# Optimization experiments

Measured on AMD Instinct MI355X. Metric: run time of the kernel, lower is better.

Reference implementation:

```python
import jax, jax.numpy as jnp
import numpy as np

N, T = 32, 1024
CIN, H, O, F2 = 64, 128, 16, 16  # F2 = 2 * FiLMed_layers
EPS = 1e-5
SLOPE = 0.01  # nn.LeakyReLU default


def _leaky(x):
    return jnp.where(x >= 0, x, SLOPE * x)


def _ln(x, gamma, beta):
    # x: (N,T,O,H); gamma,beta: (O,H) -> broadcast per channel
    mu = jnp.mean(x, axis=-1, keepdims=True)
    var = jnp.mean(jnp.square(x - mu), axis=-1, keepdims=True)
    return (x - mu) * jax.lax.rsqrt(var + EPS) * gamma + beta


def setup_inputs() -> dict:
    key = jax.random.key(0)
    ks = jax.random.split(key, 7)
    s0 = 1.0 / np.sqrt(CIN)
    s1 = 1.0 / np.sqrt(H)
    return {
        "x": jax.random.normal(ks[0], (N, T, CIN), jnp.float32),
        "W0": jax.random.uniform(ks[1], (O, H, CIN), jnp.float32, -s0, s0),
        "b0": jax.random.uniform(ks[2], (O, H), jnp.float32, -s0, s0),
        "g0": jnp.ones((O, H), jnp.float32),
        "be0": jnp.zeros((O, H), jnp.float32),
        "W1": jax.random.uniform(ks[3], (O, H, H), jnp.float32, -s1, s1),
        "b1": jax.random.uniform(ks[4], (O, H), jnp.float32, -s1, s1),
        "g1": jnp.ones((O, H), jnp.float32),
        "be1": jnp.zeros((O, H), jnp.float32),
        "W2": jax.random.uniform(ks[5], (O, F2, H), jnp.float32, -s1, s1),
        "b2": jax.random.uniform(ks[6], (O, F2), jnp.float32, -s1, s1),
    }


def reference(x, W0, b0, g0, be0, W1, b1, g1, be1, W2, b2):
    # Per-channel MLP, vectorized over the O channel axis.
    h = jnp.einsum("ntc,ohc->ntoh", x, W0) + b0          # (N,T,O,H)
    h = _ln(_leaky(h), g0, be0)
    h = jnp.einsum("ntoh,ogh->ntog", h, W1) + b1         # (N,T,O,H)
    h = _ln(_leaky(h), g1, be1)
    out = jnp.einsum("ntoh,ofh->ntof", h, W2) + b2       # (N,T,O,F2)
    out = _leaky(out)
    # torch: stack(dim=1) -> (N,O,T,F2); moveaxis(1,-1) -> (N,T,F2,O)
    return jnp.moveaxis(out, 2, 3)
```

## Files before the change

### kernel.cpp

```cpp
#include <hip/hip_runtime.h>
#include <hip/hip_bf16.h>

#define NTOK  32768
#define CIN   64
#define HDIM  128
#define O_CH  16
#define F2    16
#define SLOPE 0.01f
#define EPS   1e-5f

#define SW0_STRIDE 72
#define SW1_STRIDE 136
#define SW2_STRIDE 136
#define SH_STRIDE  136
#define SW0_OFF 0
#define SW1_OFF 9216
#define SW2_OFF (9216 + 17408)
#define WIMG_SHORTS 28800
#define SH_OFF  28800
#define SH_ROWS 256
#define SBIAS_OFF (SH_OFF + SH_ROWS * SH_STRIDE)
#define SBIAS_FLOATS 272
#define SMEM_SHORTS (SBIAS_OFF + SBIAS_FLOATS * 2)

#define WIMG_OFF   0
#define WIMG_BYTES ((size_t)O_CH * WIMG_SHORTS * 2)
#define B0F_OFF    WIMG_BYTES
#define B0F_BYTES  ((size_t)O_CH * HDIM * 4)
#define B1F_OFF    (B0F_OFF + B0F_BYTES)
#define B1F_BYTES  ((size_t)O_CH * HDIM * 4)
#define B2F_OFF    (B1F_OFF + B1F_BYTES)

typedef __attribute__((ext_vector_type(8))) short bf16x8;
typedef __attribute__((ext_vector_type(4))) short bf16x4;
typedef __attribute__((ext_vector_type(4))) float f32x4;

__device__ __forceinline__ unsigned short f2b(float f) {
  union { float f; unsigned int i; } v;
  v.f = f;
  unsigned int i = v.i;
  unsigned int r = (i + 0x7fffu + ((i >> 16) & 1u)) >> 16;
  return (unsigned short)r;
}
__device__ __forceinline__ short f2bn(float f) {
  union { __hip_bfloat16 h; short s; } v;
  v.h = __float2bfloat16(f);
  return v.s;
}
__device__ __forceinline__ float leaky(float t) {
  return fmaxf(t, SLOPE * t);
}
__device__ __forceinline__ bf16x8 cvt8(const float* __restrict__ p) {
  float4 a = *(const float4*)p;
  float4 b = *(const float4*)(p + 4);
  bf16x8 r;
  r[0] = (short)f2b(a.x); r[1] = (short)f2b(a.y);
  r[2] = (short)f2b(a.z); r[3] = (short)f2b(a.w);
  r[4] = (short)f2b(b.x); r[5] = (short)f2b(b.y);
  r[6] = (short)f2b(b.z); r[7] = (short)f2b(b.w);
  return r;
}
__device__ __forceinline__ bf16x8 cvt8s(const float* __restrict__ p,
                                        const float* __restrict__ s) {
  bf16x8 r;
#pragma unroll
  for (int i = 0; i < 8; ++i) r[i] = (short)f2b(p[i] * s[i]);
  return r;
}

__device__ __forceinline__ void leaky_ln_store(
    f32x4* acc, unsigned short* __restrict__ sh,
    int row0, int lo16, int quad) {
  float a0 = 0.f, a1 = 0.f, a2 = 0.f, a3 = 0.f;
  float c0 = 0.f, c1 = 0.f, c2 = 0.f, c3 = 0.f;
#pragma unroll
  for (int nt = 0; nt < 8; ++nt) {
    float t0 = leaky(acc[nt][0]);
    float t1 = leaky(acc[nt][1]);
    float t2 = leaky(acc[nt][2]);
    float t3 = leaky(acc[nt][3]);
    acc[nt][0] = t0; acc[nt][1] = t1; acc[nt][2] = t2; acc[nt][3] = t3;
    a0 += t0; a1 += t1; a2 += t2; a3 += t3;
    c0 = fmaf(t0, t0, c0); c1 = fmaf(t1, t1, c1);
    c2 = fmaf(t2, t2, c2); c3 = fmaf(t3, t3, c3);
  }
  float s1 = (a0 + a1) + (a2 + a3);
  float s2 = (c0 + c1) + (c2 + c3);
  s1 += __shfl_xor(s1, 16); s2 += __shfl_xor(s2, 16);
  s1 += __shfl_xor(s1, 32); s2 += __shfl_xor(s2, 32);
  float mu = s1 * (1.0f / 128.0f);
  float var = s2 * (1.0f / 128.0f) - mu * mu;
  float rs = rsqrtf(var + EPS);
  float nm = -mu * rs;
  unsigned short* dst = sh + (row0 + lo16) * SH_STRIDE + quad * 4;
#pragma unroll
  for (int nt = 0; nt < 8; ++nt) {
    bf16x4 p;
    p[0] = f2bn(fmaf(acc[nt][0], rs, nm));
    p[1] = f2bn(fmaf(acc[nt][1], rs, nm));
    p[2] = f2bn(fmaf(acc[nt][2], rs, nm));
    p[3] = f2bn(fmaf(acc[nt][3], rs, nm));
    *(bf16x4*)(dst + nt * 16) = p;
  }
}

__global__ __launch_bounds__(256) void prep(
    const float* __restrict__ W0, const float* __restrict__ b0,
    const float* __restrict__ g0, const float* __restrict__ be0,
    const float* __restrict__ W1, const float* __restrict__ b1,
    const float* __restrict__ g1, const float* __restrict__ be1,
    const float* __restrict__ W2, const float* __restrict__ b2,
    unsigned short* __restrict__ wimg,
    float* __restrict__ b0f, float* __restrict__ b1f,
    float* __restrict__ b2f) {
  const int o = blockIdx.x, tid = threadIdx.x;
  __shared__ float sg0[HDIM], sbe0[HDIM], sg1[HDIM], sbe1[HDIM];
  if (tid < 128) {
    sg0[tid]  = g0 [o * HDIM + tid];
    sbe0[tid] = be0[o * HDIM + tid];
    sg1[tid]  = g1 [o * HDIM + tid];
    sbe1[tid] = be1[o * HDIM + tid];
  }
  __syncthreads();
  unsigned short* img = wimg + (size_t)o * WIMG_SHORTS;
  const float* w0 = W0 + (size_t)o * HDIM * CIN;
  for (int c = tid; c < (HDIM * CIN) / 8; c += 256) {
    int n = c >> 3, k8 = c & 7;
    *(bf16x8*)&img[SW0_OFF + n * SW0_STRIDE + k8 * 8] = cvt8(w0 + c * 8);
  }
  const float* w1 = W1 + (size_t)o * HDIM * HDIM;
  for (int c = tid; c < (HDIM * HDIM) / 8; c += 256) {
    int n = c >> 4, k8 = c & 15;
    *(bf16x8*)&img[SW1_OFF + n * SW1_STRIDE + k8 * 8] =
        cvt8s(w1 + c * 8, sg0 + k8 * 8);
  }
  const float* w2 = W2 + (size_t)o * F2 * HDIM;
  for (int c = tid; c < (F2 * HDIM) / 8; c += 256) {
    int n = c >> 4, k8 = c & 15;
    *(bf16x8*)&img[SW2_OFF + n * SW2_STRIDE + k8 * 8] =
        cvt8s(w2 + c * 8, sg1 + k8 * 8);
  }
  if (tid < 128) {
    b0f[o * HDIM + tid] = b0[o * HDIM + tid];
    float d = 0.f;
    const float* w1r = w1 + (size_t)tid * HDIM;
    for (int k = 0; k < HDIM; ++k) d += w1r[k] * sbe0[k];
    b1f[o * HDIM + tid] = b1[o * HDIM + tid] + d;
  } else if (tid < 144) {
    int f = tid - 128;
    float d = 0.f;
    const float* w2r = w2 + (size_t)f * HDIM;
    for (int k = 0; k < HDIM; ++k) d += w2r[k] * sbe1[k];
    b2f[o * F2 + f] = b2[o * F2 + f] + d;
  }
}

__global__ __launch_bounds__(1024)
__attribute__((amdgpu_waves_per_eu(4, 4))) void film_main(
    const float* __restrict__ x,
    const unsigned short* __restrict__ wimg,
    const float* __restrict__ b0f, const float* __restrict__ b1f,
    const float* __restrict__ b2f,
    float* __restrict__ out) {
  __shared__ unsigned short smem[SMEM_SHORTS];
  const int tid = threadIdx.x;
  const int c   = blockIdx.x & 7;
  const int o   = (blockIdx.x >> 3) & 15;
  const int q   = blockIdx.x >> 7;
  const int tok0 = (q * 8 + c) * 1024;

  {
    const bf16x8* src = (const bf16x8*)(wimg + (size_t)o * WIMG_SHORTS);
    for (int i = tid; i < WIMG_SHORTS / 8; i += 1024)
      *(bf16x8*)&smem[i * 8] = src[i];
  }
  float* sbias = (float*)&smem[SBIAS_OFF];
  if (tid < 128)      sbias[tid] = b0f[o * HDIM + tid];
  else if (tid < 256) sbias[tid] = b1f[o * HDIM + (tid - 128)];
  else if (tid < 272) sbias[tid] = b2f[o * F2 + (tid - 256)];

  const int lane = tid & 63;
  const int wave = tid >> 6;
  const int lo16 = lane & 15;
  const int quad = lane >> 4;
  const int row0 = wave * 16;
  const float* sb0 = sbias;
  const float* sb1 = sbias + HDIM;
  const float* sb2 = sbias + 2 * HDIM;

  const int tbase = tok0 + wave * 64;
  const float* xw = x + (size_t)(tbase + lo16) * CIN + quad * 8;
  float4 xa0 = *(const float4*)(xw);
  float4 xb0 = *(const float4*)(xw + 4);
  float4 xa1 = *(const float4*)(xw + 32);
  float4 xb1 = *(const float4*)(xw + 36);
  __syncthreads();

  for (int mt = 0; mt < 4; ++mt) {
    const int trow = tbase + mt * 16;

    bf16x8 bx0, bx1;
    bx0[0] = f2bn(xa0.x); bx0[1] = f2bn(xa0.y);
    bx0[2] = f2bn(xa0.z); bx0[3] = f2bn(xa0.w);
    bx0[4] = f2bn(xb0.x); bx0[5] = f2bn(xb0.y);
    bx0[6] = f2bn(xb0.z); bx0[7] = f2bn(xb0.w);
    bx1[0] = f2bn(xa1.x); bx1[1] = f2bn(xa1.y);
    bx1[2] = f2bn(xa1.z); bx1[3] = f2bn(xa1.w);
    bx1[4] = f2bn(xb1.x); bx1[5] = f2bn(xb1.y);
    bx1[6] = f2bn(xb1.z); bx1[7] = f2bn(xb1.w);
    if (mt < 3) {
      const float* xn = xw + (size_t)(mt + 1) * 16 * CIN;
      xa0 = *(const float4*)(xn);
      xb0 = *(const float4*)(xn + 4);
      xa1 = *(const float4*)(xn + 32);
      xb1 = *(const float4*)(xn + 36);
    }

    f32x4 acc[8];
#pragma unroll
    for (int nt = 0; nt < 8; ++nt)
      acc[nt] = *(const f32x4*)(sb0 + nt * 16 + quad * 4);
#pragma unroll
    for (int nt = 0; nt < 8; ++nt) {
      bf16x8 a = *(const bf16x8*)
          &smem[SW0_OFF + (nt * 16 + lo16) * SW0_STRIDE + quad * 8];
      acc[nt] = __builtin_amdgcn_mfma_f32_16x16x32_bf16(a, bx0, acc[nt], 0, 0, 0);
    }
#pragma unroll
    for (int nt = 0; nt < 8; ++nt) {
      bf16x8 a = *(const bf16x8*)
          &smem[SW0_OFF + (nt * 16 + lo16) * SW0_STRIDE + 32 + quad * 8];
      acc[nt] = __builtin_amdgcn_mfma_f32_16x16x32_bf16(a, bx1, acc[nt], 0, 0, 0);
    }
    leaky_ln_store(acc, smem + SH_OFF, row0, lo16, quad);

#pragma unroll
    for (int nt = 0; nt < 8; ++nt)
      acc[nt] = *(const f32x4*)(sb1 + nt * 16 + quad * 4);
#pragma unroll
    for (int ks = 0; ks < 4; ++ks) {
      bf16x8 bh = *(const bf16x8*)
          &smem[SH_OFF + (row0 + lo16) * SH_STRIDE + ks * 32 + quad * 8];
#pragma unroll
      for (int nt = 0; nt < 8; ++nt) {
        bf16x8 a = *(const bf16x8*)
            &smem[SW1_OFF + (nt * 16 + lo16) * SW1_STRIDE + ks * 32 + quad * 8];
        acc[nt] = __builtin_amdgcn_mfma_f32_16x16x32_bf16(a, bh, acc[nt], 0, 0, 0);
      }
    }
    leaky_ln_store(acc, smem + SH_OFF, row0, lo16, quad);

    f32x4 acc2 = *(const f32x4*)(sb2 + quad * 4);
#pragma unroll
    for (int ks = 0; ks < 4; ++ks) {
      bf16x8 bh = *(const bf16x8*)
          &smem[SH_OFF + (row0 + lo16) * SH_STRIDE + ks * 32 + quad * 8];
      bf16x8 a = *(const bf16x8*)
          &smem[SW2_OFF + lo16 * SW2_STRIDE + ks * 32 + quad * 8];
      acc2 = __builtin_amdgcn_mfma_f32_16x16x32_bf16(a, bh, acc2, 0, 0, 0);
    }
    {
      const size_t tb = (size_t)(trow + lo16) * (F2 * O_CH);
#pragma unroll
      for (int r = 0; r < 4; ++r)
        out[tb + (quad * 4 + r) * O_CH + o] = leaky(acc2[r]);
    }
  }
}

extern "C" void kernel_launch(void* const* d_in, const int* in_sizes, int n_in,
                              void* d_out, int out_size, void* d_ws, size_t ws_size,
                              hipStream_t stream) {
  (void)in_sizes; (void)n_in; (void)out_size; (void)ws_size;
  const float* x   = (const float*)d_in[0];
  const float* W0  = (const float*)d_in[1];
  const float* b0  = (const float*)d_in[2];
  const float* g0  = (const float*)d_in[3];
  const float* be0 = (const float*)d_in[4];
  const float* W1  = (const float*)d_in[5];
  const float* b1  = (const float*)d_in[6];
  const float* g1  = (const float*)d_in[7];
  const float* be1 = (const float*)d_in[8];
  const float* W2  = (const float*)d_in[9];
  const float* b2  = (const float*)d_in[10];

  unsigned short* wimg = (unsigned short*)((char*)d_ws + WIMG_OFF);
  float* b0f = (float*)((char*)d_ws + B0F_OFF);
  float* b1f = (float*)((char*)d_ws + B1F_OFF);
  float* b2f = (float*)((char*)d_ws + B2F_OFF);

  prep<<<dim3(O_CH), dim3(256), 0, stream>>>(
      W0, b0, g0, be0, W1, b1, g1, be1, W2, b2, wimg, b0f, b1f, b2f);
  film_main<<<dim3(O_CH * (NTOK / 1024)), dim3(1024), 0, stream>>>(
      x, wimg, b0f, b1f, b2f, (float*)d_out);
}
```

Measured before the change: 146.4 us.

## Fuse weight prep into main kernel, converting weights per block in-kernel

Removes the separate prep kernel that built a bf16 weight image and folded biases in workspace. Each main-kernel block now loads the fp32 weights for its channel, applies the LayerNorm gamma scaling, converts to bf16 into shared memory, and computes the beta-folded biases with a shuffle-reduced dot product. This drops one launch and the serial dependency on a 16-block prep kernel. In exchange, every block re-reads twice as many bytes of fp32 weights and redoes the conversion work, which is redundant across the 32 blocks that share a channel.

```diff
diff --git a/kernel.cpp b/kernel.cpp
--- a/kernel.cpp
+++ b/kernel.cpp
@@ -21,15 +21,9 @@
 #define SH_ROWS 256
 #define SBIAS_OFF (SH_OFF + SH_ROWS * SH_STRIDE)
 #define SBIAS_FLOATS 272
-#define SMEM_SHORTS (SBIAS_OFF + SBIAS_FLOATS * 2)
-
-#define WIMG_OFF   0
-#define WIMG_BYTES ((size_t)O_CH * WIMG_SHORTS * 2)
-#define B0F_OFF    WIMG_BYTES
-#define B0F_BYTES  ((size_t)O_CH * HDIM * 4)
-#define B1F_OFF    (B0F_OFF + B0F_BYTES)
-#define B1F_BYTES  ((size_t)O_CH * HDIM * 4)
-#define B2F_OFF    (B1F_OFF + B1F_BYTES)
+#define SGB_OFF (SBIAS_OFF + SBIAS_FLOATS * 2)
+#define SGB_FLOATS 512
+#define SMEM_SHORTS (SGB_OFF + SGB_FLOATS * 2)
 
 typedef __attribute__((ext_vector_type(8))) short bf16x8;
 typedef __attribute__((ext_vector_type(4))) short bf16x4;
@@ -104,63 +98,14 @@
   }
 }
 
-__global__ __launch_bounds__(256) void prep(
+__global__ __launch_bounds__(1024)
+__attribute__((amdgpu_waves_per_eu(4, 4))) void film_main(
+    const float* __restrict__ x,
     const float* __restrict__ W0, const float* __restrict__ b0,
     const float* __restrict__ g0, const float* __restrict__ be0,
     const float* __restrict__ W1, const float* __restrict__ b1,
     const float* __restrict__ g1, const float* __restrict__ be1,
     const float* __restrict__ W2, const float* __restrict__ b2,
-    unsigned short* __restrict__ wimg,
-    float* __restrict__ b0f, float* __restrict__ b1f,
-    float* __restrict__ b2f) {
-  const int o = blockIdx.x, tid = threadIdx.x;
-  __shared__ float sg0[HDIM], sbe0[HDIM], sg1[HDIM], sbe1[HDIM];
-  if (tid < 128) {
-    sg0[tid]  = g0 [o * HDIM + tid];
-    sbe0[tid] = be0[o * HDIM + tid];
-    sg1[tid]  = g1 [o * HDIM + tid];
-    sbe1[tid] = be1[o * HDIM + tid];
-  }
-  __syncthreads();
-  unsigned short* img = wimg + (size_t)o * WIMG_SHORTS;
-  const float* w0 = W0 + (size_t)o * HDIM * CIN;
-  for (int c = tid; c < (HDIM * CIN) / 8; c += 256) {
-    int n = c >> 3, k8 = c & 7;
-    *(bf16x8*)&img[SW0_OFF + n * SW0_STRIDE + k8 * 8] = cvt8(w0 + c * 8);
-  }
-  const float* w1 = W1 + (size_t)o * HDIM * HDIM;
-  for (int c = tid; c < (HDIM * HDIM) / 8; c += 256) {
-    int n = c >> 4, k8 = c & 15;
-    *(bf16x8*)&img[SW1_OFF + n * SW1_STRIDE + k8 * 8] =
-        cvt8s(w1 + c * 8, sg0 + k8 * 8);
-  }
-  const float* w2 = W2 + (size_t)o * F2 * HDIM;
-  for (int c = tid; c < (F2 * HDIM) / 8; c += 256) {
-    int n = c >> 4, k8 = c & 15;
-    *(bf16x8*)&img[SW2_OFF + n * SW2_STRIDE + k8 * 8] =
-        cvt8s(w2 + c * 8, sg1 + k8 * 8);
-  }
-  if (tid < 128) {
-    b0f[o * HDIM + tid] = b0[o * HDIM + tid];
-    float d = 0.f;
-    const float* w1r = w1 + (size_t)tid * HDIM;
-    for (int k = 0; k < HDIM; ++k) d += w1r[k] * sbe0[k];
-    b1f[o * HDIM + tid] = b1[o * HDIM + tid] + d;
-  } else if (tid < 144) {
-    int f = tid - 128;
-    float d = 0.f;
-    const float* w2r = w2 + (size_t)f * HDIM;
-    for (int k = 0; k < HDIM; ++k) d += w2r[k] * sbe1[k];
-    b2f[o * F2 + f] = b2[o * F2 + f] + d;
-  }
-}
-
-__global__ __launch_bounds__(1024)
-__attribute__((amdgpu_waves_per_eu(4, 4))) void film_main(
-    const float* __restrict__ x,
-    const unsigned short* __restrict__ wimg,
-    const float* __restrict__ b0f, const float* __restrict__ b1f,
-    const float* __restrict__ b2f,
     float* __restrict__ out) {
   __shared__ unsigned short smem[SMEM_SHORTS];
   const int tid = threadIdx.x;
@@ -169,15 +114,58 @@
   const int q   = blockIdx.x >> 7;
   const int tok0 = (q * 8 + c) * 1024;
 
+  float* sbias = (float*)&smem[SBIAS_OFF];
+  float* sgb   = (float*)&smem[SGB_OFF];
+  float* sg0v  = sgb;
+  float* sbe0v = sgb + 128;
+  float* sg1v  = sgb + 256;
+  float* sbe1v = sgb + 384;
+
+  if (tid < 128)      sg0v [tid]       = g0 [o * HDIM + tid];
+  else if (tid < 256) sbe0v[tid - 128] = be0[o * HDIM + (tid - 128)];
+  else if (tid < 384) sg1v [tid - 256] = g1 [o * HDIM + (tid - 256)];
+  else if (tid < 512) sbe1v[tid - 384] = be1[o * HDIM + (tid - 384)];
+  __syncthreads();
+
+  const float* w0 = W0 + (size_t)o * HDIM * CIN;
+  const float* w1 = W1 + (size_t)o * HDIM * HDIM;
+  const float* w2 = W2 + (size_t)o * F2 * HDIM;
   {
-    const bf16x8* src = (const bf16x8*)(wimg + (size_t)o * WIMG_SHORTS);
-    for (int i = tid; i < WIMG_SHORTS / 8; i += 1024)
-      *(bf16x8*)&smem[i * 8] = src[i];
-  }
-  float* sbias = (float*)&smem[SBIAS_OFF];
-  if (tid < 128)      sbias[tid] = b0f[o * HDIM + tid];
-  else if (tid < 256) sbias[tid] = b1f[o * HDIM + (tid - 128)];
-  else if (tid < 272) sbias[tid] = b2f[o * F2 + (tid - 256)];
+    int cc = tid, n = cc >> 3, k8 = cc & 7;
+    *(bf16x8*)&smem[SW0_OFF + n * SW0_STRIDE + k8 * 8] = cvt8(w0 + cc * 8);
+  }
+#pragma unroll
+  for (int rep = 0; rep < 2; ++rep) {
+    int cc = tid + rep * 1024, n = cc >> 4, k8 = cc & 15;
+    *(bf16x8*)&smem[SW1_OFF + n * SW1_STRIDE + k8 * 8] =
+        cvt8s(w1 + cc * 8, sg0v + k8 * 8);
+  }
+  if (tid < 256) {
+    int cc = tid, n = cc >> 4, k8 = cc & 15;
+    *(bf16x8*)&smem[SW2_OFF + n * SW2_STRIDE + k8 * 8] =
+        cvt8s(w2 + cc * 8, sg1v + k8 * 8);
+  }
+  if (tid < 128) sbias[tid] = b0[o * HDIM + tid];
+  {
+    int h = tid >> 3, seg = tid & 7;
+    const float* w1r = w1 + (size_t)h * HDIM + seg * 16;
+    const float* bev = sbe0v + seg * 16;
+    float p = 0.f;
+#pragma unroll
+    for (int k = 0; k < 16; ++k) p = fmaf(w1r[k], bev[k], p);
+    p += __shfl_xor(p, 1); p += __shfl_xor(p, 2); p += __shfl_xor(p, 4);
+    if (seg == 0) sbias[HDIM + h] = b1[o * HDIM + h] + p;
+  }
+  if (tid < 128) {
+    int f = tid >> 3, seg = tid & 7;
+    const float* w2r = w2 + (size_t)f * HDIM + seg * 16;
+    const float* bev = sbe1v + seg * 16;
+    float p = 0.f;
+#pragma unroll
+    for (int k = 0; k < 16; ++k) p = fmaf(w2r[k], bev[k], p);
+    p += __shfl_xor(p, 1); p += __shfl_xor(p, 2); p += __shfl_xor(p, 4);
+    if (seg == 0) sbias[2 * HDIM + f] = b2[o * F2 + f] + p;
+  }
 
   const int lane = tid & 63;
   const int wave = tid >> 6;
@@ -271,7 +259,7 @@
 extern "C" void kernel_launch(void* const* d_in, const int* in_sizes, int n_in,
                               void* d_out, int out_size, void* d_ws, size_t ws_size,
                               hipStream_t stream) {
-  (void)in_sizes; (void)n_in; (void)out_size; (void)ws_size;
+  (void)in_sizes; (void)n_in; (void)out_size; (void)d_ws; (void)ws_size;
   const float* x   = (const float*)d_in[0];
   const float* W0  = (const float*)d_in[1];
   const float* b0  = (const float*)d_in[2];
@@ -284,13 +272,6 @@
   const float* W2  = (const float*)d_in[9];
   const float* b2  = (const float*)d_in[10];
 
-  unsigned short* wimg = (unsigned short*)((char*)d_ws + WIMG_OFF);
-  float* b0f = (float*)((char*)d_ws + B0F_OFF);
-  float* b1f = (float*)((char*)d_ws + B1F_OFF);
-  float* b2f = (float*)((char*)d_ws + B2F_OFF);
-
-  prep<<<dim3(O_CH), dim3(256), 0, stream>>>(
-      W0, b0, g0, be0, W1, b1, g1, be1, W2, b2, wimg, b0f, b1f, b2f);
   film_main<<<dim3(O_CH * (NTOK / 1024)), dim3(1024), 0, stream>>>(
-      x, wimg, b0f, b1f, b2f, (float*)d_out);
-}
+      x, W0, b0, g0, be0, W1, b1, g1, be1, W2, b2, (float*)d_out);
+}
```

Result: no change. 146.6 us (+0.1%).
